# Kernel tuning notes

Measured on AMD Instinct MI355X. Metric: run time of the kernel, lower is better.

## Reference

```python
import jax, jax.numpy as jnp
import numpy as np

CHANNELS = 256

def setup_inputs() -> dict:
    key = jax.random.key(0)
    ks = jax.random.split(key, 7)
    B, C, N = 4, CHANNELS, 4096
    scale = 1.0 / np.sqrt(C)
    x = jax.random.normal(ks[0], (B, C, N), dtype=jnp.float32)
    Wq = jax.random.normal(ks[1], (C, C), dtype=jnp.float32) * scale
    bq = jax.random.normal(ks[2], (C,), dtype=jnp.float32) * 0.01
    Wk = jax.random.normal(ks[3], (C, C), dtype=jnp.float32) * scale
    bk = jax.random.normal(ks[4], (C,), dtype=jnp.float32) * 0.01
    Wv = jax.random.normal(ks[5], (C, C), dtype=jnp.float32) * scale
    bv = jax.random.normal(ks[6], (C,), dtype=jnp.float32) * 0.01
    return {"x": x, "Wq": Wq, "bq": bq, "Wk": Wk, "bk": bk, "Wv": Wv, "bv": bv}

def reference(x, Wq, bq, Wk, bk, Wv, bv):
    # x: [B, C, N]; 1x1 Conv1d == channel-mixing matmul
    C = x.shape[1]
    Q = jnp.einsum('oc,bcn->bon', Wq, x) + bq[None, :, None]   # [B, C, N]
    K = jnp.einsum('oc,bcn->bon', Wk, x) + bk[None, :, None]   # [B, C, N]
    V = jnp.einsum('oc,bcn->bon', Wv, x) + bv[None, :, None]   # [B, C, N]
    # attn[b, i, j] = softmax_j( Q[:, i]^T K[:, j] / sqrt(C) )
    scores = jnp.einsum('bci,bcj->bij', Q, K) / jnp.sqrt(jnp.asarray(C, x.dtype))
    attn = jax.nn.softmax(scores, axis=-1)                     # [B, N, N]
    context = jnp.einsum('bij,bcj->bci', attn, V)              # [B, C, N]
    return x + context
```

## Files before the change

kernel.cpp:

```cpp
#include <hip/hip_runtime.h>
#include <stdint.h>

#define B_ 4
#define C_ 256
#define N_ 4096
#define JS 4

typedef unsigned short u16;
typedef __attribute__((ext_vector_type(4))) float f32x4;
typedef __attribute__((ext_vector_type(16))) float f32x16;
typedef __attribute__((ext_vector_type(8))) short bf16x8;
typedef __attribute__((ext_vector_type(4))) int i32x4;

__device__ __forceinline__ u16 f2bf(float f) {
    uint32_t u = __float_as_uint(f);
    u += 0x7fffu + ((u >> 16) & 1u);
    return (u16)(u >> 16);
}
__device__ __forceinline__ float bf2f(u16 v) {
    uint32_t u = ((uint32_t)v) << 16;
    return __uint_as_float(u);
}
__device__ __forceinline__ uint32_t pkbf(float a, float b) {
    uint32_t ua = __float_as_uint(a) + 0x8000u;
    uint32_t ub = __float_as_uint(b) + 0x8000u;
    return (ua >> 16) | (ub & 0xffff0000u);
}

#if defined(__has_builtin)
#if __has_builtin(__builtin_amdgcn_global_load_lds)
#define HAVE_GLL 1
#endif
#endif

#ifdef HAVE_GLL
__device__ __forceinline__ void g2l16(const u16* g, u16* lbase, int lane) {
    (void)lane;
    __builtin_amdgcn_global_load_lds(
        (__attribute__((address_space(1))) void*)(uintptr_t)g,
        (__attribute__((address_space(3))) void*)lbase, 16, 0, 0);
}
#else
__device__ __forceinline__ void g2l16(const u16* g, u16* lbase, int lane) {
    *(i32x4*)(lbase + lane * 8) = *(const i32x4*)g;
}
#endif

__global__ __launch_bounds__(256) void wconv_kernel(
    const float* __restrict__ Wq, const float* __restrict__ Wk,
    const float* __restrict__ Wv, u16* __restrict__ Wb) {
    int id = blockIdx.x * 256 + threadIdx.x;
    const float* src = (id < 65536) ? Wq : ((id < 131072) ? Wk : Wv);
    Wb[id] = f2bf(src[id & 65535]);
}

__global__ __launch_bounds__(256, 2) void qkv_kernel(
    const float* __restrict__ x, const u16* __restrict__ Wb,
    const float* __restrict__ bq, const float* __restrict__ bk,
    const float* __restrict__ bv,
    u16* __restrict__ Qt, u16* __restrict__ Kt, u16* __restrict__ Vt) {
    const int XTS = 264;
    __shared__ __align__(16) u16 xT[32 * XTS];

    int blk = blockIdx.x;
    int n0  = (blk & 127) << 5;
    int b   = blk >> 7;
    int tid = threadIdx.x;
    int lane = tid & 63;
    int w = tid >> 6;
    int l31 = lane & 31;
    int h = lane >> 5;

    {
        int c0 = tid >> 3;
        int nq = (tid & 7) << 2;
        const float* xb = x + ((size_t)b * C_ + c0) * N_ + n0 + nq;
        #pragma unroll
        for (int p = 0; p < 8; ++p) {
            f32x4 v = *(const f32x4*)(xb + (size_t)32 * N_ * p);
            int cc = c0 + 32 * p;
            xT[(nq + 0) * XTS + cc] = f2bf(v[0]);
            xT[(nq + 1) * XTS + cc] = f2bf(v[1]);
            xT[(nq + 2) * XTS + cc] = f2bf(v[2]);
            xT[(nq + 3) * XTS + cc] = f2bf(v[3]);
        }
    }
    __syncthreads();

    bf16x8 xf[16];
    #pragma unroll
    for (int ks = 0; ks < 16; ++ks)
        xf[ks] = *(const bf16x8*)(&xT[l31 * XTS + 16 * ks + 8 * h]);

    #pragma unroll
    for (int mat = 0; mat < 2; ++mat) {
        const u16* W = Wb + mat * 65536;
        const float* bias = mat ? bk : bq;
        u16* dst = mat ? Kt : Qt;
        f32x16 acc0, acc1;
        #pragma unroll
        for (int r = 0; r < 16; ++r) { acc0[r] = 0.f; acc1[r] = 0.f; }
        const u16* wr0 = W + (size_t)(64 * w + l31) * 256 + 8 * h;
        const u16* wr1 = W + (size_t)(64 * w + 32 + l31) * 256 + 8 * h;
        #pragma unroll
        for (int ks = 0; ks < 16; ++ks) {
            bf16x8 wf0 = *(const bf16x8*)(wr0 + 16 * ks);
            bf16x8 wf1 = *(const bf16x8*)(wr1 + 16 * ks);
            acc0 = __builtin_amdgcn_mfma_f32_32x32x16_bf16(xf[ks], wf0, acc0, 0, 0, 0);
            acc1 = __builtin_amdgcn_mfma_f32_32x32x16_bf16(xf[ks], wf1, acc1, 0, 0, 0);
        }
        #pragma unroll
        for (int ot = 0; ot < 2; ++ot) {
            const f32x16& a = ot ? acc1 : acc0;
            int o = 64 * w + 32 * ot + l31;
            float bo = bias[o];
            #pragma unroll
            for (int g = 0; g < 4; ++g)
                #pragma unroll
                for (int r = 0; r < 4; ++r) {
                    int n = 8 * g + 4 * h + r;
                    int oc = mat ? ((((o >> 3) ^ n) << 3) | (o & 7)) : o;
                    dst[((size_t)b * N_ + n0 + n) * C_ + oc] = f2bf(a[4 * g + r] + bo);
                }
        }
    }

    {
        const u16* W = Wb + 2 * 65536;
        f32x16 acc0, acc1;
        #pragma unroll
        for (int r = 0; r < 16; ++r) { acc0[r] = 0.f; acc1[r] = 0.f; }
        const u16* wr0 = W + (size_t)(64 * w + l31) * 256 + 8 * h;
        const u16* wr1 = W + (size_t)(64 * w + 32 + l31) * 256 + 8 * h;
        #pragma unroll
        for (int ks = 0; ks < 16; ++ks) {
            bf16x8 wf0 = *(const bf16x8*)(wr0 + 16 * ks);
            bf16x8 wf1 = *(const bf16x8*)(wr1 + 16 * ks);
            acc0 = __builtin_amdgcn_mfma_f32_32x32x16_bf16(wf0, xf[ks], acc0, 0, 0, 0);
            acc1 = __builtin_amdgcn_mfma_f32_32x32x16_bf16(wf1, xf[ks], acc1, 0, 0, 0);
        }
        int nj = n0 + l31;
        int tb = nj & ~63;
        int local = nj & 63;
        #pragma unroll
        for (int mt = 0; mt < 2; ++mt) {
            const f32x16& a = mt ? acc1 : acc0;
            #pragma unroll
            for (int g = 0; g < 4; ++g)
                #pragma unroll
                for (int r = 0; r < 4; ++r) {
                    int o = 64 * w + 32 * mt + 8 * g + 4 * h + r;
                    int njs = tb | ((((local >> 3) ^ (o & 7)) << 3) | (local & 7));
                    Vt[((size_t)b * C_ + o) * N_ + njs] = f2bf(a[4 * g + r] + bv[o]);
                }
        }
    }
}

__device__ __forceinline__ void stage64(const u16* Kb, const u16* Vb, int j0,
                                        u16* ksd, u16* vsd, int w, int lane) {
    const u16* kg = Kb + (size_t)(j0 + 8 * w) * C_ + lane * 8;
    u16* kdb = ksd + 8 * w * 256;
    #pragma unroll
    for (int rr = 0; rr < 4; ++rr)
        g2l16(kg + rr * 512, kdb + rr * 512, lane);
    const u16* vg = Vb + (size_t)(32 * w + (lane >> 3)) * N_ + j0 + (lane & 7) * 8;
    u16* vdb = vsd + 32 * w * 64;
    #pragma unroll
    for (int rr = 0; rr < 4; ++rr)
        g2l16(vg + (size_t)8 * rr * N_, vdb + rr * 512, lane);
}

__global__ __launch_bounds__(512, 2) void attn_kernel(
    const u16* __restrict__ Qt, const u16* __restrict__ Kt,
    const u16* __restrict__ Vt, u16* __restrict__ Op,
    float* __restrict__ lArr) {
    __shared__ __align__(16) u16 Ksh[2 * 64 * 256];
    __shared__ __align__(16) u16 Vsh[2 * 256 * 64];

    int blk = blockIdx.x;
    int it = blk & 15;
    int b  = (blk >> 4) & 3;
    int s  = blk >> 6;
    int i0 = it << 8;
    int tid = threadIdx.x;
    int lane = tid & 63;
    int w = tid >> 6;
    int l31 = lane & 31;
    int h = lane >> 5;

    bf16x8 qf[16];
    {
        const u16* qrow = Qt + ((size_t)b * N_ + i0 + 32 * w + l31) * C_ + 8 * h;
        #pragma unroll
        for (int ks = 0; ks < 16; ++ks) qf[ks] = *(const bf16x8*)(qrow + 16 * ks);
    }

    f32x16 oacc[8];
    #pragma unroll
    for (int mt = 0; mt < 8; ++mt)
        #pragma unroll
        for (int r = 0; r < 16; ++r) oacc[mt][r] = 0.f;
    float l_run = 0.f;

    const float sconst = 0.0625f * 1.44269504088896340736f;
    const u16* Kb = Kt + (size_t)b * N_ * C_;
    const u16* Vb = Vt + (size_t)b * C_ * N_;
    int jbase = s * (N_ / JS);

    stage64(Kb, Vb, jbase, Ksh, Vsh, w, lane);
    __syncthreads();

    for (int jt = 0; jt < N_ / (64 * JS); ++jt) {
        int cur = jt & 1;
        const u16* ks_ = Ksh + cur * 64 * 256;
        const u16* vs_ = Vsh + cur * 256 * 64;

        if (jt + 1 < N_ / (64 * JS))
            stage64(Kb, Vb, jbase + (jt + 1) * 64,
                    Ksh + (cur ^ 1) * 64 * 256, Vsh + (cur ^ 1) * 256 * 64, w, lane);

        f32x16 st0, st1;
        #pragma unroll
        for (int r = 0; r < 16; ++r) { st0[r] = 0.f; st1[r] = 0.f; }
        #pragma unroll
        for (int ks = 0; ks < 16; ++ks) {
            int kc = ((2 * ks + h) ^ l31) << 3;
            bf16x8 kf0 = *(const bf16x8*)(ks_ + l31 * 256 + kc);
            bf16x8 kf1 = *(const bf16x8*)(ks_ + (32 + l31) * 256 + kc);
            st0 = __builtin_amdgcn_mfma_f32_32x32x16_bf16(kf0, qf[ks], st0, 0, 0, 0);
            st1 = __builtin_amdgcn_mfma_f32_32x32x16_bf16(kf1, qf[ks], st1, 0, 0, 0);
        }

        float psum = 0.f;
        uint32_t pd[16];
        #pragma unroll
        for (int u = 0; u < 8; ++u) {
            const f32x16& stv = (u < 4) ? st0 : st1;
            int g = u & 3;
            #pragma unroll
            for (int d = 0; d < 2; ++d) {
                float p0 = exp2f(stv[4 * g + 2 * d + 0] * sconst);
                float p1 = exp2f(stv[4 * g + 2 * d + 1] * sconst);
                psum += p0 + p1;
                pd[u * 2 + d] = pkbf(p0, p1);
            }
        }
        psum += __shfl_xor(psum, 32);
        l_run += psum;

        bf16x8 pf[4];
        #pragma unroll
        for (int ks2 = 0; ks2 < 4; ++ks2) {
            uint32_t oA0 = pd[4 * ks2 + 0], oA1 = pd[4 * ks2 + 1];
            uint32_t oB0 = pd[4 * ks2 + 2], oB1 = pd[4 * ks2 + 3];
            uint32_t sn0 = h ? oA0 : oB0, sn1 = h ? oA1 : oB1;
            uint32_t rc0 = (uint32_t)__shfl_xor((int)sn0, 32);
            uint32_t rc1 = (uint32_t)__shfl_xor((int)sn1, 32);
            uint32_t ow0 = h ? oB0 : oA0, ow1 = h ? oB1 : oA1;
            i32x4 fr;
            fr[0] = (int)(h ? rc0 : ow0);
            fr[1] = (int)(h ? rc1 : ow1);
            fr[2] = (int)(h ? ow0 : rc0);
            fr[3] = (int)(h ? ow1 : rc1);
            pf[ks2] = *(bf16x8*)&fr;
        }

        #pragma unroll
        for (int ks2 = 0; ks2 < 4; ++ks2) {
            int vc = ((2 * ks2 + h) ^ (l31 & 7)) << 3;
            #pragma unroll
            for (int mt = 0; mt < 8; ++mt) {
                bf16x8 vf = *(const bf16x8*)(vs_ + (32 * mt + l31) * 64 + vc);
                oacc[mt] = __builtin_amdgcn_mfma_f32_32x32x16_bf16(vf, pf[ks2], oacc[mt], 0, 0, 0);
            }
        }
        __syncthreads();
    }

    int i = i0 + 32 * w + l31;
    u16* ob = Op + ((size_t)(s * B_ + b) * C_) * N_ + i;
    #pragma unroll
    for (int mt = 0; mt < 8; ++mt)
        #pragma unroll
        for (int g = 0; g < 4; ++g)
            #pragma unroll
            for (int r = 0; r < 4; ++r) {
                int c = 32 * mt + 8 * g + r + 4 * h;
                ob[(size_t)c * N_] = f2bf(oacc[mt][4 * g + r]);
            }
    if (h == 0) lArr[(size_t)(s * B_ + b) * N_ + i] = l_run;
}

__global__ __launch_bounds__(256) void merge_kernel(
    const float* __restrict__ x, const u16* __restrict__ Op,
    const float* __restrict__ lArr, float* __restrict__ out) {
    int blk = blockIdx.x;
    int ch = blk & 1;
    int ib = (blk >> 1) & 63;
    int b  = blk >> 7;
    int i  = ib * 64 + (threadIdx.x & 63);
    int csub = threadIdx.x >> 6;

    float L = 0.f;
    #pragma unroll
    for (int s = 0; s < JS; ++s) L += lArr[(size_t)(s * B_ + b) * N_ + i];
    float rL = 1.0f / L;

    for (int cc = 0; cc < 32; ++cc) {
        int c = ch * 128 + csub * 32 + cc;
        size_t xi = ((size_t)b * C_ + c) * N_ + i;
        float acc = 0.f;
        #pragma unroll
        for (int s = 0; s < JS; ++s)
            acc += bf2f(Op[((size_t)(s * B_ + b) * C_ + c) * N_ + i]);
        out[xi] = fmaf(acc, rL, x[xi]);
    }
}

extern "C" void kernel_launch(void* const* d_in, const int* in_sizes, int n_in,
                              void* d_out, int out_size, void* d_ws, size_t ws_size,
                              hipStream_t stream) {
    const float* x  = (const float*)d_in[0];
    const float* Wq = (const float*)d_in[1];
    const float* bq = (const float*)d_in[2];
    const float* Wk = (const float*)d_in[3];
    const float* bk = (const float*)d_in[4];
    const float* Wv = (const float*)d_in[5];
    const float* bv = (const float*)d_in[6];
    float* out = (float*)d_out;

    u16* Wb = (u16*)d_ws;
    u16* Qt = Wb + 3 * 65536;
    u16* Kt = Qt + (size_t)B_ * N_ * C_;
    u16* Vt = Kt + (size_t)B_ * N_ * C_;
    u16* Op = Vt + (size_t)B_ * N_ * C_;
    float* lArr = (float*)(Op + (size_t)JS * B_ * C_ * N_);

    wconv_kernel<<<768, 256, 0, stream>>>(Wq, Wk, Wv, Wb);
    qkv_kernel<<<512, 256, 0, stream>>>(x, Wb, bq, bk, bv, Qt, Kt, Vt);
    attn_kernel<<<256, 512, 0, stream>>>(Qt, Kt, Vt, Op, lArr);
    merge_kernel<<<512, 256, 0, stream>>>(x, Op, lArr, out);
}
```

Before: 202.6 us.

## Shrink attention key tile to 32 with 4-stage LDS ring and software-pipelined QK

Changes the attention main loop from 64-key tiles with double buffering to 32-key tiles with a 4-deep shared-memory ring, prefetching three tiles ahead. The QK^T MFMA for the next tile is issued before the PV MFMAs of the current tile, so score computation overlaps the softmax and accumulation work. The V layout swizzle is adjusted to match the 32-wide tile, and the merge loop gets an unroll pragma. Smaller tiles double the loop iterations and barriers, and the extra in-flight score tile adds register pressure.

```diff
diff --git a/kernel.cpp b/kernel.cpp
--- a/kernel.cpp
+++ b/kernel.cpp
@@ -140,8 +140,6 @@
             acc1 = __builtin_amdgcn_mfma_f32_32x32x16_bf16(wf1, xf[ks], acc1, 0, 0, 0);
         }
         int nj = n0 + l31;
-        int tb = nj & ~63;
-        int local = nj & 63;
         #pragma unroll
         for (int mt = 0; mt < 2; ++mt) {
             const f32x16& a = mt ? acc1 : acc0;
@@ -150,33 +148,33 @@
                 #pragma unroll
                 for (int r = 0; r < 4; ++r) {
                     int o = 64 * w + 32 * mt + 8 * g + 4 * h + r;
-                    int njs = tb | ((((local >> 3) ^ (o & 7)) << 3) | (local & 7));
+                    int njs = (nj & ~31) | ((((nj & 31) >> 3) ^ ((o >> 1) & 3)) << 3) | (nj & 7);
                     Vt[((size_t)b * C_ + o) * N_ + njs] = f2bf(a[4 * g + r] + bv[o]);
                 }
         }
     }
 }
 
-__device__ __forceinline__ void stage64(const u16* Kb, const u16* Vb, int j0,
+__device__ __forceinline__ void stage32(const u16* Kb, const u16* Vb, int j0,
                                         u16* ksd, u16* vsd, int w, int lane) {
-    const u16* kg = Kb + (size_t)(j0 + 8 * w) * C_ + lane * 8;
-    u16* kdb = ksd + 8 * w * 256;
-    #pragma unroll
-    for (int rr = 0; rr < 4; ++rr)
-        g2l16(kg + rr * 512, kdb + rr * 512, lane);
-    const u16* vg = Vb + (size_t)(32 * w + (lane >> 3)) * N_ + j0 + (lane & 7) * 8;
-    u16* vdb = vsd + 32 * w * 64;
-    #pragma unroll
-    for (int rr = 0; rr < 4; ++rr)
-        g2l16(vg + (size_t)8 * rr * N_, vdb + rr * 512, lane);
+    #pragma unroll
+    for (int rr = 0; rr < 2; ++rr) {
+        const u16* kg = Kb + (size_t)(j0 + 4 * w + 2 * rr + (lane >> 5)) * C_ + (lane & 31) * 8;
+        g2l16(kg, ksd + (4 * w + 2 * rr) * 256, lane);
+    }
+    #pragma unroll
+    for (int rr = 0; rr < 2; ++rr) {
+        const u16* vg = Vb + (size_t)(32 * w + 16 * rr + (lane >> 2)) * N_ + j0 + (lane & 3) * 8;
+        g2l16(vg, vsd + (32 * w + 16 * rr) * 32, lane);
+    }
 }
 
 __global__ __launch_bounds__(512, 2) void attn_kernel(
     const u16* __restrict__ Qt, const u16* __restrict__ Kt,
     const u16* __restrict__ Vt, u16* __restrict__ Op,
     float* __restrict__ lArr) {
-    __shared__ __align__(16) u16 Ksh[2 * 64 * 256];
-    __shared__ __align__(16) u16 Vsh[2 * 256 * 64];
+    __shared__ __align__(16) u16 Ksh[4 * 32 * 256];
+    __shared__ __align__(16) u16 Vsh[4 * 256 * 32];
 
     int blk = blockIdx.x;
     int it = blk & 15;
@@ -207,57 +205,51 @@
     const u16* Kb = Kt + (size_t)b * N_ * C_;
     const u16* Vb = Vt + (size_t)b * C_ * N_;
     int jbase = s * (N_ / JS);
-
-    stage64(Kb, Vb, jbase, Ksh, Vsh, w, lane);
+    const int T = N_ / (32 * JS);
+
+    stage32(Kb, Vb, jbase + 0 * 32, Ksh + 0 * 32 * 256, Vsh + 0 * 256 * 32, w, lane);
+    stage32(Kb, Vb, jbase + 1 * 32, Ksh + 1 * 32 * 256, Vsh + 1 * 256 * 32, w, lane);
+    stage32(Kb, Vb, jbase + 2 * 32, Ksh + 2 * 32 * 256, Vsh + 2 * 256 * 32, w, lane);
     __syncthreads();
 
-    for (int jt = 0; jt < N_ / (64 * JS); ++jt) {
-        int cur = jt & 1;
-        const u16* ks_ = Ksh + cur * 64 * 256;
-        const u16* vs_ = Vsh + cur * 256 * 64;
-
-        if (jt + 1 < N_ / (64 * JS))
-            stage64(Kb, Vb, jbase + (jt + 1) * 64,
-                    Ksh + (cur ^ 1) * 64 * 256, Vsh + (cur ^ 1) * 256 * 64, w, lane);
-
-        f32x16 st0, st1;
-        #pragma unroll
-        for (int r = 0; r < 16; ++r) { st0[r] = 0.f; st1[r] = 0.f; }
-        #pragma unroll
-        for (int ks = 0; ks < 16; ++ks) {
-            int kc = ((2 * ks + h) ^ l31) << 3;
-            bf16x8 kf0 = *(const bf16x8*)(ks_ + l31 * 256 + kc);
-            bf16x8 kf1 = *(const bf16x8*)(ks_ + (32 + l31) * 256 + kc);
-            st0 = __builtin_amdgcn_mfma_f32_32x32x16_bf16(kf0, qf[ks], st0, 0, 0, 0);
-            st1 = __builtin_amdgcn_mfma_f32_32x32x16_bf16(kf1, qf[ks], st1, 0, 0, 0);
-        }
+    f32x16 st;
+    #pragma unroll
+    for (int r = 0; r < 16; ++r) st[r] = 0.f;
+    #pragma unroll
+    for (int ks = 0; ks < 16; ++ks) {
+        int kc = ((2 * ks + h) ^ l31) << 3;
+        bf16x8 kf = *(const bf16x8*)(Ksh + l31 * 256 + kc);
+        st = __builtin_amdgcn_mfma_f32_32x32x16_bf16(kf, qf[ks], st, 0, 0, 0);
+    }
+
+    for (int jt = 0; jt < T; ++jt) {
+        if (jt + 3 < T)
+            stage32(Kb, Vb, jbase + (jt + 3) * 32,
+                    Ksh + ((jt + 3) & 3) * 32 * 256, Vsh + ((jt + 3) & 3) * 256 * 32, w, lane);
 
         float psum = 0.f;
-        uint32_t pd[16];
-        #pragma unroll
-        for (int u = 0; u < 8; ++u) {
-            const f32x16& stv = (u < 4) ? st0 : st1;
-            int g = u & 3;
+        uint32_t pd[8];
+        #pragma unroll
+        for (int g = 0; g < 4; ++g)
             #pragma unroll
             for (int d = 0; d < 2; ++d) {
-                float p0 = exp2f(stv[4 * g + 2 * d + 0] * sconst);
-                float p1 = exp2f(stv[4 * g + 2 * d + 1] * sconst);
+                float p0 = exp2f(st[4 * g + 2 * d + 0] * sconst);
+                float p1 = exp2f(st[4 * g + 2 * d + 1] * sconst);
                 psum += p0 + p1;
-                pd[u * 2 + d] = pkbf(p0, p1);
+                pd[2 * g + d] = pkbf(p0, p1);
             }
-        }
         psum += __shfl_xor(psum, 32);
         l_run += psum;
 
-        bf16x8 pf[4];
-        #pragma unroll
-        for (int ks2 = 0; ks2 < 4; ++ks2) {
-            uint32_t oA0 = pd[4 * ks2 + 0], oA1 = pd[4 * ks2 + 1];
-            uint32_t oB0 = pd[4 * ks2 + 2], oB1 = pd[4 * ks2 + 3];
-            uint32_t sn0 = h ? oA0 : oB0, sn1 = h ? oA1 : oB1;
+        bf16x8 pf[2];
+        #pragma unroll
+        for (int ks2 = 0; ks2 < 2; ++ks2) {
+            int bo = 4 * ks2 + 2 * h;
+            int so = 4 * ks2 + 2 - 2 * h;
+            uint32_t sn0 = pd[so], sn1 = pd[so + 1];
             uint32_t rc0 = (uint32_t)__shfl_xor((int)sn0, 32);
             uint32_t rc1 = (uint32_t)__shfl_xor((int)sn1, 32);
-            uint32_t ow0 = h ? oB0 : oA0, ow1 = h ? oB1 : oA1;
+            uint32_t ow0 = pd[bo], ow1 = pd[bo + 1];
             i32x4 fr;
             fr[0] = (int)(h ? rc0 : ow0);
             fr[1] = (int)(h ? rc1 : ow1);
@@ -266,13 +258,30 @@
             pf[ks2] = *(bf16x8*)&fr;
         }
 
-        #pragma unroll
-        for (int ks2 = 0; ks2 < 4; ++ks2) {
-            int vc = ((2 * ks2 + h) ^ (l31 & 7)) << 3;
-            #pragma unroll
-            for (int mt = 0; mt < 8; ++mt) {
-                bf16x8 vf = *(const bf16x8*)(vs_ + (32 * mt + l31) * 64 + vc);
-                oacc[mt] = __builtin_amdgcn_mfma_f32_32x32x16_bf16(vf, pf[ks2], oacc[mt], 0, 0, 0);
+        if (jt + 1 < T) {
+            const u16* ksb = Ksh + ((jt + 1) & 3) * 32 * 256;
+            f32x16 stn;
+            #pragma unroll
+            for (int r = 0; r < 16; ++r) stn[r] = 0.f;
+            #pragma unroll
+            for (int ks = 0; ks < 16; ++ks) {
+                int kc = ((2 * ks + h) ^ l31) << 3;
+                bf16x8 kf = *(const bf16x8*)(ksb + l31 * 256 + kc);
+                stn = __builtin_amdgcn_mfma_f32_32x32x16_bf16(kf, qf[ks], stn, 0, 0, 0);
+            }
+            st = stn;
+        }
+
+        {
+            const u16* vsb = Vsh + (jt & 3) * 256 * 32;
+            #pragma unroll
+            for (int ks2 = 0; ks2 < 2; ++ks2) {
+                int vc = ((2 * ks2 + h) ^ ((l31 >> 1) & 3)) << 3;
+                #pragma unroll
+                for (int mt = 0; mt < 8; ++mt) {
+                    bf16x8 vf = *(const bf16x8*)(vsb + (32 * mt + l31) * 32 + vc);
+                    oacc[mt] = __builtin_amdgcn_mfma_f32_32x32x16_bf16(vf, pf[ks2], oacc[mt], 0, 0, 0);
+                }
             }
         }
         __syncthreads();
@@ -307,6 +316,7 @@
     for (int s = 0; s < JS; ++s) L += lArr[(size_t)(s * B_ + b) * N_ + i];
     float rL = 1.0f / L;
 
+    #pragma unroll 4
     for (int cc = 0; cc < 32; ++cc) {
         int c = ch * 128 + csub * 32 + cc;
         size_t xi = ((size_t)b * C_ + c) * N_ + i;
```

Result: slower. 227.6 us (+12.4%).
